# Optimization experiments

Hardware: AMD Instinct MI355X
Metric: run time of the kernel (lower is better)

The kernel has to match this reference:

```python
import jax, jax.numpy as jnp
import numpy as np

NUM_GROUPS = 32
EPS = 1e-5


def group_norm(x, weight, bias):
    # x: [B, C, H, W]; normalize per (group, sample) over channels-in-group and spatial dims
    B, C, H, W = x.shape
    g = x.reshape(B, NUM_GROUPS, C // NUM_GROUPS, H, W)
    mean = g.mean(axis=(2, 3, 4), keepdims=True)
    var = g.var(axis=(2, 3, 4), keepdims=True)
    g = (g - mean) * jax.lax.rsqrt(var + EPS)
    g = g.reshape(B, C, H, W)
    return g * weight[None, :, None, None] + bias[None, :, None, None]


def conv1x1(x, w, b):
    # x: [B, C, H, W], w: [O, C] (1x1 conv kernel squeezed), b: [O]
    return jnp.einsum('bchw,oc->bohw', x, w) + b[None, :, None, None]


def setup_inputs() -> dict:
    key = jax.random.key(0)
    ks = jax.random.split(key, 6)
    B, C, H, W = 16, 512, 64, 64
    scale = 1.0 / np.sqrt(C)
    x = jax.random.normal(ks[0], (B, C, H, W), dtype=jnp.float32)
    return {
        'x': x,
        'gn_weight': jnp.ones((C,), jnp.float32),
        'gn_bias': jnp.zeros((C,), jnp.float32),
        'wq': jax.random.normal(ks[1], (C, C), jnp.float32) * scale,
        'bq': jnp.zeros((C,), jnp.float32),
        'wk': jax.random.normal(ks[2], (C, C), jnp.float32) * scale,
        'bk': jnp.zeros((C,), jnp.float32),
        'wv': jax.random.normal(ks[3], (C, C), jnp.float32) * scale,
        'bv': jnp.zeros((C,), jnp.float32),
        'wo': jax.random.normal(ks[4], (C, C), jnp.float32) * (scale * 1e-5),
        'bo': jnp.zeros((C,), jnp.float32),
    }


def reference(x, gn_weight, gn_bias, wq, bq, wk, bk, wv, bv, wo, bo):
    B, C, H, W = x.shape
    h = group_norm(x, gn_weight, gn_bias)
    q = conv1x1(h, wq, bq)  # [B, C, H, W]
    k = conv1x1(h, wk, bk)
    v = conv1x1(h, wv, bv)
    q = q.transpose(0, 2, 3, 1).reshape(B, H * W, C)   # [B, HW, C]
    kf = k.reshape(B, C, H * W)                        # [B, C, HW]
    w = jnp.einsum('bnc,bcm->bnm', q, kf) * (C ** -0.5)  # [B, HW, HW]
    w = jax.nn.softmax(w, axis=-1)
    vf = v.transpose(0, 2, 3, 1).reshape(B, H * W, C)
    h = jnp.einsum('bnm,bmc->bnc', w, vf)              # [B, HW, C]
    h = h.reshape(B, H, W, C).transpose(0, 3, 1, 2)    # [B, C, H, W]
    h = conv1x1(h, wo, bo)
    return x + h
```

## Files before the change

### kernel.cpp

```cpp
#include <hip/hip_runtime.h>
#include <stdint.h>

typedef __bf16 bf16x8 __attribute__((ext_vector_type(8)));
typedef float  f32x4  __attribute__((ext_vector_type(4)));
typedef unsigned short ushortx8 __attribute__((ext_vector_type(8)));
typedef unsigned short ushortx4 __attribute__((ext_vector_type(4)));

#define DEVI __device__ __forceinline__

DEVI unsigned short f2bf(float f) {
  union { float f; unsigned int u; } v; v.f = f;
  unsigned int r = v.u + 0x7fffu + ((v.u >> 16) & 1u);
  return (unsigned short)(r >> 16);
}
DEVI float bf2f(unsigned short h) {
  union { unsigned int u; float f; } v; v.u = ((unsigned int)h) << 16;
  return v.f;
}

DEVI void gl_lds16(const unsigned short* g, unsigned short* l) {
  __builtin_amdgcn_global_load_lds(
      (__attribute__((address_space(1))) unsigned int*)g,
      (__attribute__((address_space(3))) unsigned int*)l,
      16, 0, 0);
}

DEVI void raw_barrier() {
  asm volatile("" ::: "memory");
  __builtin_amdgcn_s_barrier();
  asm volatile("" ::: "memory");
}
#define WAITCNT_VM4 0x0F74
#define WAITCNT_VM0 0x0F70

DEVI void store_out(float* p, float v) { *p = v; }
DEVI void store_out(unsigned short* p, float v) { *p = f2bf(v); }

__global__ __launch_bounds__(256) void gn_stats(const float* __restrict__ x,
                                                float* __restrict__ stats) {
  const int bg = blockIdx.x;
  const float* p = x + (size_t)bg * 65536;
  const int tid = threadIdx.x;
  float s = 0.f, ss = 0.f;
#pragma unroll 4
  for (int i = 0; i < 64; ++i) {
    float4 v = *(const float4*)(p + (((size_t)i * 256 + tid) << 2));
    s  += v.x + v.y + v.z + v.w;
    ss += v.x * v.x + v.y * v.y + v.z * v.z + v.w * v.w;
  }
  for (int off = 32; off; off >>= 1) { s += __shfl_xor(s, off); ss += __shfl_xor(ss, off); }
  __shared__ float rs[4], rss[4];
  const int lane = tid & 63, wave = tid >> 6;
  if (lane == 0) { rs[wave] = s; rss[wave] = ss; }
  __syncthreads();
  if (tid == 0) {
    float S1 = rs[0] + rs[1] + rs[2] + rs[3];
    float S2 = rss[0] + rss[1] + rss[2] + rss[3];
    float mean = S1 * (1.f / 65536.f);
    float var  = S2 * (1.f / 65536.f) - mean * mean;
    stats[bg * 2 + 0] = mean;
    stats[bg * 2 + 1] = rsqrtf(var + 1e-5f);
  }
}

__global__ __launch_bounds__(256) void gn_apply(const float* __restrict__ x,
                                                const float* __restrict__ stats,
                                                const float* __restrict__ gamma,
                                                const float* __restrict__ beta,
                                                unsigned short* __restrict__ h_t) {
  __shared__ alignas(16) unsigned short tile[64 * 136];
  const int tid = threadIdx.x;
  const int t0 = blockIdx.x * 64;
  const int c0 = blockIdx.y * 128;
  const int b  = blockIdx.z;
  const float* xb = x + ((size_t)b * 512 + c0) * 4096 + t0;
#pragma unroll
  for (int j = 0; j < 8; ++j) {
    int f = tid + j * 256;
    int r = f >> 4;
    int tc = (f & 15) << 2;
    float4 v = *(const float4*)(xb + (size_t)r * 4096 + tc);
    int ch = c0 + r;
    int g = ch >> 4;
    float mean = stats[((size_t)b * 32 + g) * 2 + 0];
    float rstd = stats[((size_t)b * 32 + g) * 2 + 1];
    float ga = gamma[ch] * rstd;
    float be = beta[ch] - mean * ga;
    tile[(tc + 0) * 136 + r] = f2bf(v.x * ga + be);
    tile[(tc + 1) * 136 + r] = f2bf(v.y * ga + be);
    tile[(tc + 2) * 136 + r] = f2bf(v.z * ga + be);
    tile[(tc + 3) * 136 + r] = f2bf(v.w * ga + be);
  }
  __syncthreads();
  unsigned short* hb = h_t + (size_t)b * 4096 * 512;
#pragma unroll
  for (int j = 0; j < 4; ++j) {
    int f = tid + j * 256;
    int tok = f >> 4;
    int cc = (f & 15) << 3;
    ushortx8 v = *(const ushortx8*)&tile[tok * 136 + cc];
    *(ushortx8*)(hb + (size_t)(t0 + tok) * 512 + c0 + cc) = v;
  }
}

__global__ __launch_bounds__(256) void cvt_f32_bf16(const float* __restrict__ s,
                                                    unsigned short* __restrict__ d) {
  int i = (blockIdx.x * 256 + threadIdx.x) * 4;
  float4 v = *(const float4*)(s + i);
  ushortx4 o;
  o[0] = f2bf(v.x); o[1] = f2bf(v.y); o[2] = f2bf(v.z); o[3] = f2bf(v.w);
  *(ushortx4*)(d + i) = o;
}

template <int BIAS_MODE, int RESID, typename OT>
__global__ __launch_bounds__(256) void gemm_nt(
    const unsigned short* __restrict__ A, const unsigned short* __restrict__ B,
    OT* __restrict__ D, const float* __restrict__ bias,
    const float* __restrict__ resid, int M, int N, int K,
    long long sA, long long sB, long long sD, long long sR, float alpha) {
  __shared__ alignas(16) unsigned short As[2][128 * 32];
  __shared__ alignas(16) unsigned short Bs[2][128 * 32];

  const int tid = threadIdx.x;
  const int bz = blockIdx.x, bn = blockIdx.y, bm = blockIdx.z;
  const unsigned short* Ab = A + (size_t)bz * sA + (size_t)bm * 128 * K;
  const unsigned short* Bb = B + (size_t)bz * sB + (size_t)bn * 128 * K;

  const int lane = tid & 63, wave = tid >> 6;
  const int wr = (wave >> 1) * 64, wc = (wave & 1) * 64;
  const int quad = lane >> 4, ln = lane & 15;

  const int r0 = tid >> 2, r1 = (tid + 256) >> 2;
  const int cc = (tid & 3) << 3;

  unsigned short* l0a[2] = { &As[0][(size_t)tid << 3], &As[1][(size_t)tid << 3] };
  unsigned short* l1a[2] = { &As[0][(size_t)(tid + 256) << 3], &As[1][(size_t)(tid + 256) << 3] };
  unsigned short* l0b[2] = { &Bs[0][(size_t)tid << 3], &Bs[1][(size_t)tid << 3] };
  unsigned short* l1b[2] = { &Bs[0][(size_t)(tid + 256) << 3], &Bs[1][(size_t)(tid + 256) << 3] };

  f32x4 acc[4][4] = {};

  const int KT = K >> 5;

  {
    const unsigned short* ag = Ab;
    const unsigned short* bg = Bb;
    gl_lds16(ag + (size_t)r0 * K + cc, l0a[0]);
    gl_lds16(ag + (size_t)r1 * K + cc, l1a[0]);
    gl_lds16(bg + (size_t)r0 * K + cc, l0b[0]);
    gl_lds16(bg + (size_t)r1 * K + cc, l1b[0]);
  }

  int kt = 0;
  for (; kt < KT - 1; ++kt) {
    const int cur = kt & 1, nxt = cur ^ 1;
    {
      const size_t k0 = (size_t)(kt + 1) << 5;
      const unsigned short* ag = Ab + k0;
      const unsigned short* bg = Bb + k0;
      gl_lds16(ag + (size_t)r0 * K + cc, l0a[nxt]);
      gl_lds16(ag + (size_t)r1 * K + cc, l1a[nxt]);
      gl_lds16(bg + (size_t)r0 * K + cc, l0b[nxt]);
      gl_lds16(bg + (size_t)r1 * K + cc, l1b[nxt]);
    }
    __builtin_amdgcn_s_waitcnt(WAITCNT_VM4);
    raw_barrier();

    bf16x8 af[4], bq[4];
#pragma unroll
    for (int mi = 0; mi < 4; ++mi)
      af[mi] = *(const bf16x8*)&As[cur][(wr + mi * 16 + ln) * 32 + quad * 8];
#pragma unroll
    for (int ni = 0; ni < 4; ++ni)
      bq[ni] = *(const bf16x8*)&Bs[cur][(wc + ni * 16 + ln) * 32 + quad * 8];
#pragma unroll
    for (int mi = 0; mi < 4; ++mi)
#pragma unroll
      for (int ni = 0; ni < 4; ++ni)
        acc[mi][ni] = __builtin_amdgcn_mfma_f32_16x16x32_bf16(af[mi], bq[ni],
                                                              acc[mi][ni], 0, 0, 0);
    raw_barrier();
  }

  {
    const int cur = kt & 1;
    __builtin_amdgcn_s_waitcnt(WAITCNT_VM0);
    raw_barrier();
    bf16x8 af[4], bq[4];
#pragma unroll
    for (int mi = 0; mi < 4; ++mi)
      af[mi] = *(const bf16x8*)&As[cur][(wr + mi * 16 + ln) * 32 + quad * 8];
#pragma unroll
    for (int ni = 0; ni < 4; ++ni)
      bq[ni] = *(const bf16x8*)&Bs[cur][(wc + ni * 16 + ln) * 32 + quad * 8];
#pragma unroll
    for (int mi = 0; mi < 4; ++mi)
#pragma unroll
      for (int ni = 0; ni < 4; ++ni)
        acc[mi][ni] = __builtin_amdgcn_mfma_f32_16x16x32_bf16(af[mi], bq[ni],
                                                              acc[mi][ni], 0, 0, 0);
  }

  OT* Db = D + (size_t)bz * sD;
  const float* Rb = RESID ? (resid + (size_t)bz * sR) : nullptr;
#pragma unroll
  for (int mi = 0; mi < 4; ++mi) {
#pragma unroll
    for (int ni = 0; ni < 4; ++ni) {
#pragma unroll
      for (int r = 0; r < 4; ++r) {
        int row = bm * 128 + wr + mi * 16 + quad * 4 + r;
        int col = bn * 128 + wc + ni * 16 + ln;
        float v = acc[mi][ni][r] * alpha;
        if (BIAS_MODE == 1) v += bias[row];
        if (BIAS_MODE == 2) v += bias[col];
        size_t idx = (size_t)row * N + col;
        if (RESID) v += Rb[idx];
        store_out(&Db[idx], v);
      }
    }
  }
}

__global__ __launch_bounds__(256) void softmax_rows(unsigned short* __restrict__ S) {
  const int tid = threadIdx.x;
  unsigned short* p = S + (size_t)blockIdx.x * 4096 + tid * 16;
  ushortx8 u0 = *(const ushortx8*)p;
  ushortx8 u1 = *(const ushortx8*)(p + 8);
  float v[16];
#pragma unroll
  for (int i = 0; i < 8; ++i) { v[i] = bf2f(u0[i]); v[i + 8] = bf2f(u1[i]); }
  float m = v[0];
#pragma unroll
  for (int i = 1; i < 16; ++i) m = fmaxf(m, v[i]);
  for (int off = 32; off; off >>= 1) m = fmaxf(m, __shfl_xor(m, off));
  __shared__ float red[4];
  __shared__ float red2[4];
  const int lane = tid & 63, wave = tid >> 6;
  if (lane == 0) red[wave] = m;
  __syncthreads();
  m = fmaxf(fmaxf(red[0], red[1]), fmaxf(red[2], red[3]));
  float s = 0.f;
#pragma unroll
  for (int i = 0; i < 16; ++i) { v[i] = __expf(v[i] - m); s += v[i]; }
  for (int off = 32; off; off >>= 1) s += __shfl_xor(s, off);
  if (lane == 0) red2[wave] = s;
  __syncthreads();
  s = red2[0] + red2[1] + red2[2] + red2[3];
  float inv = 1.f / s;
#pragma unroll
  for (int i = 0; i < 8; ++i) { u0[i] = f2bf(v[i] * inv); u1[i] = f2bf(v[i + 8] * inv); }
  *(ushortx8*)p = u0;
  *(ushortx8*)(p + 8) = u1;
}

extern "C" void kernel_launch(void* const* d_in, const int* in_sizes, int n_in,
                              void* d_out, int out_size, void* d_ws, size_t ws_size,
                              hipStream_t stream) {
  const float* x   = (const float*)d_in[0];
  const float* gnw = (const float*)d_in[1];
  const float* gnb = (const float*)d_in[2];
  const float* wq  = (const float*)d_in[3];
  const float* bq  = (const float*)d_in[4];
  const float* wk  = (const float*)d_in[5];
  const float* bk  = (const float*)d_in[6];
  const float* wv  = (const float*)d_in[7];
  const float* bv  = (const float*)d_in[8];
  const float* wo  = (const float*)d_in[9];
  const float* bo  = (const float*)d_in[10];
  float* out = (float*)d_out;

  const size_t EB = 2097152;

  char* base = (char*)d_ws;
  unsigned short* h_t  = (unsigned short*)base;
  unsigned short* wqb  = (unsigned short*)(base + 67108864);
  unsigned short* wkb  = wqb + 262144;
  unsigned short* wvb  = wkb + 262144;
  unsigned short* wob  = wvb + 262144;
  float*          stats = (float*)(base + 69206016);
  char*           dyn   = base + 69210112;
  size_t rem = ws_size > 69210112 ? ws_size - 69210112 : 0;

  int nb = 1;
  if      (rem >= (size_t)16 * 46137344) nb = 16;
  else if (rem >= (size_t)8  * 46137344) nb = 8;
  else if (rem >= (size_t)4  * 46137344) nb = 4;
  else if (rem >= (size_t)2  * 46137344) nb = 2;

  unsigned short* q  = (unsigned short*)dyn;
  unsigned short* kb = q  + (size_t)nb * EB;
  unsigned short* vb = kb + (size_t)nb * EB;
  unsigned short* Sb = (unsigned short*)(dyn + (size_t)nb * 3 * 4194304);
  unsigned short* attn = q;

  gn_stats<<<512, 256, 0, stream>>>(x, stats);
  gn_apply<<<dim3(64, 4, 16), 256, 0, stream>>>(x, stats, gnw, gnb, h_t);
  cvt_f32_bf16<<<256, 256, 0, stream>>>(wq, wqb);
  cvt_f32_bf16<<<256, 256, 0, stream>>>(wk, wkb);
  cvt_f32_bf16<<<256, 256, 0, stream>>>(wv, wvb);
  cvt_f32_bf16<<<256, 256, 0, stream>>>(wo, wob);

  const float sm_scale = 0.044194173824159216f;

  for (int b0 = 0; b0 < 16; b0 += nb) {
    const unsigned short* hc = h_t + (size_t)b0 * EB;
    gemm_nt<2, 0, unsigned short><<<dim3(nb, 4, 32), 256, 0, stream>>>(
        hc, wqb, q, bq, nullptr, 4096, 512, 512, (long long)EB, 0, (long long)EB, 0, 1.f);
    gemm_nt<2, 0, unsigned short><<<dim3(nb, 4, 32), 256, 0, stream>>>(
        hc, wkb, kb, bk, nullptr, 4096, 512, 512, (long long)EB, 0, (long long)EB, 0, 1.f);
    gemm_nt<1, 0, unsigned short><<<dim3(nb, 32, 4), 256, 0, stream>>>(
        wvb, hc, vb, bv, nullptr, 512, 4096, 512, 0, (long long)EB, (long long)EB, 0, 1.f);
    gemm_nt<0, 0, unsigned short><<<dim3(nb, 32, 32), 256, 0, stream>>>(
        q, kb, Sb, nullptr, nullptr, 4096, 4096, 512,
        (long long)EB, (long long)EB, 16777216LL, 0, sm_scale);
    softmax_rows<<<nb * 4096, 256, 0, stream>>>(Sb);
    gemm_nt<0, 0, unsigned short><<<dim3(nb, 4, 32), 256, 0, stream>>>(
        Sb, vb, attn, nullptr, nullptr, 4096, 512, 4096,
        16777216LL, (long long)EB, (long long)EB, 0, 1.f);
    gemm_nt<1, 1, float><<<dim3(nb, 32, 4), 256, 0, stream>>>(
        wob, attn, out + (size_t)b0 * EB, bo, x + (size_t)b0 * EB,
        512, 4096, 512, 0, (long long)EB, (long long)EB, (long long)EB, 1.f);
  }
}
```

Measured before the change: 1.522 ms.

## Replace 128x128 GEMM with 256x256-tile 8-wave kernel using swizzled LDS pipeline

```diff
diff --git a/kernel.cpp b/kernel.cpp
--- a/kernel.cpp
+++ b/kernel.cpp
@@ -30,8 +30,9 @@
   __builtin_amdgcn_s_barrier();
   asm volatile("" ::: "memory");
 }
-#define WAITCNT_VM4 0x0F74
-#define WAITCNT_VM0 0x0F70
+#define WAITCNT_VM4    0x0F74
+#define WAITCNT_VM0    0x0F70
+#define WAITCNT_LGKM0  0xC07F
 
 DEVI void store_out(float* p, float v) { *p = v; }
 DEVI void store_out(unsigned short* p, float v) { *p = f2bf(v); }
@@ -113,105 +114,159 @@
 }
 
 template <int BIAS_MODE, int RESID, typename OT>
-__global__ __launch_bounds__(256) void gemm_nt(
+__global__ __launch_bounds__(512, 2) void gemm_nt_256(
     const unsigned short* __restrict__ A, const unsigned short* __restrict__ B,
     OT* __restrict__ D, const float* __restrict__ bias,
     const float* __restrict__ resid, int M, int N, int K,
     long long sA, long long sB, long long sD, long long sR, float alpha) {
-  __shared__ alignas(16) unsigned short As[2][128 * 32];
-  __shared__ alignas(16) unsigned short Bs[2][128 * 32];
+  __shared__ alignas(128) char sm[131072];
+  char* const sA0 = sm;
+  char* const sB0 = sm + 32768;
+  char* const sA1 = sm + 65536;
+  char* const sB1 = sm + 98304;
 
   const int tid = threadIdx.x;
   const int bz = blockIdx.x, bn = blockIdx.y, bm = blockIdx.z;
-  const unsigned short* Ab = A + (size_t)bz * sA + (size_t)bm * 128 * K;
-  const unsigned short* Bb = B + (size_t)bz * sB + (size_t)bn * 128 * K;
-
-  const int lane = tid & 63, wave = tid >> 6;
-  const int wr = (wave >> 1) * 64, wc = (wave & 1) * 64;
-  const int quad = lane >> 4, ln = lane & 15;
-
-  const int r0 = tid >> 2, r1 = (tid + 256) >> 2;
-  const int cc = (tid & 3) << 3;
-
-  unsigned short* l0a[2] = { &As[0][(size_t)tid << 3], &As[1][(size_t)tid << 3] };
-  unsigned short* l1a[2] = { &As[0][(size_t)(tid + 256) << 3], &As[1][(size_t)(tid + 256) << 3] };
-  unsigned short* l0b[2] = { &Bs[0][(size_t)tid << 3], &Bs[1][(size_t)tid << 3] };
-  unsigned short* l1b[2] = { &Bs[0][(size_t)(tid + 256) << 3], &Bs[1][(size_t)(tid + 256) << 3] };
-
-  f32x4 acc[4][4] = {};
-
-  const int KT = K >> 5;
-
+  const unsigned short* Ab = A + (size_t)bz * sA + (size_t)bm * 256 * K;
+  const unsigned short* Bb = B + (size_t)bz * sB + (size_t)bn * 256 * K;
+
+  const int lane = tid & 63;
+  const int ln = lane & 15, quad = lane >> 4;
+  const int wave = tid >> 6;
+  const int wm = wave >> 2, wn = wave & 3;
+
+  const int prow = tid >> 3;
+  const unsigned ks = (unsigned)((tid & 7) ^ (prow & 7));
+  const unsigned srcoff = (unsigned)prow * (unsigned)K + ks * 8u;
+  const unsigned ldst = (unsigned)tid * 16u;
+
+  const int aro = (wm * 128 + ln) * 128;
+  const int bro = (wn * 64 + ln) * 128;
+  const int sl0 = ((quad ^ (ln & 7)) << 4);
+  const int sl1 = (((4 + quad) ^ (ln & 7)) << 4);
+
+  f32x4 acc[8][4] = {};
+  bf16x8 a0[8], a1[8], b0[4], b1[4];
+
+#define STAGE(G, SMp, h, ktv) do {                                                   \
+    const unsigned short* _g = (G) + (unsigned)(h) * 128u * (unsigned)K +            \
+                               (unsigned)(ktv) * 64u + srcoff;                       \
+    gl_lds16(_g, (unsigned short*)((SMp) + (h) * 16384 + ldst));                     \
+    gl_lds16(_g + (size_t)64 * K, (unsigned short*)((SMp) + (h) * 16384 + 8192 + ldst)); \
+  } while (0)
+
+#define RD_A(SMp, SL, dst) do { _Pragma("unroll")                                    \
+    for (int _mf = 0; _mf < 8; ++_mf)                                                \
+      dst[_mf] = *(const bf16x8*)((SMp) + aro + _mf * 2048 + (SL)); } while (0)
+#define RD_B(SMp, SL, dst) do { _Pragma("unroll")                                    \
+    for (int _nf = 0; _nf < 4; ++_nf)                                                \
+      dst[_nf] = *(const bf16x8*)((SMp) + bro + _nf * 2048 + (SL)); } while (0)
+
+#define MM(AF, BF, N0) do {                                                          \
+    __builtin_amdgcn_s_setprio(1);                                                   \
+    _Pragma("unroll")                                                                \
+    for (int _mf = 0; _mf < 8; ++_mf) {                                              \
+      acc[_mf][(N0)]     = __builtin_amdgcn_mfma_f32_16x16x32_bf16(AF[_mf], BF[(N0)],     acc[_mf][(N0)],     0, 0, 0); \
+      acc[_mf][(N0) + 1] = __builtin_amdgcn_mfma_f32_16x16x32_bf16(AF[_mf], BF[(N0) + 1], acc[_mf][(N0) + 1], 0, 0, 0); \
+    }                                                                                \
+    __builtin_amdgcn_s_setprio(0);                                                   \
+  } while (0)
+
+  STAGE(Ab, sA0, 0, 0); STAGE(Ab, sA0, 1, 0);
+  STAGE(Bb, sB0, 0, 0); STAGE(Bb, sB0, 1, 0);
+  STAGE(Ab, sA1, 0, 1); STAGE(Ab, sA1, 1, 1);
+  __builtin_amdgcn_s_waitcnt(WAITCNT_VM4);
+  raw_barrier();
+
+  const int NI = K >> 7;
+  int kt0 = 0;
+  for (int i = 0; i < NI - 1; ++i, kt0 += 2) {
+    RD_A(sA0, sl0, a0); RD_B(sB0, sl0, b0);
+    STAGE(Bb, sB1, 0, kt0 + 1);
+    raw_barrier();
+    MM(a0, b0, 0);
+    raw_barrier();
+    RD_A(sA0, sl1, a1); RD_B(sB0, sl1, b1);
+    STAGE(Bb, sB1, 1, kt0 + 1);
+    raw_barrier();
+    MM(a0, b0, 2);
+    __builtin_amdgcn_s_waitcnt(WAITCNT_LGKM0);
+    raw_barrier();
+    STAGE(Ab, sA0, 0, kt0 + 2);
+    raw_barrier();
+    MM(a1, b1, 0);
+    raw_barrier();
+    STAGE(Ab, sA0, 1, kt0 + 2);
+    raw_barrier();
+    MM(a1, b1, 2);
+    __builtin_amdgcn_s_waitcnt(WAITCNT_VM4);
+    raw_barrier();
+    RD_A(sA1, sl0, a0); RD_B(sB1, sl0, b0);
+    STAGE(Bb, sB0, 0, kt0 + 2);
+    raw_barrier();
+    MM(a0, b0, 0);
+    raw_barrier();
+    RD_A(sA1, sl1, a1); RD_B(sB1, sl1, b1);
+    STAGE(Bb, sB0, 1, kt0 + 2);
+    raw_barrier();
+    MM(a0, b0, 2);
+    __builtin_amdgcn_s_waitcnt(WAITCNT_LGKM0);
+    raw_barrier();
+    STAGE(Ab, sA1, 0, kt0 + 3);
+    raw_barrier();
+    MM(a1, b1, 0);
+    raw_barrier();
+    STAGE(Ab, sA1, 1, kt0 + 3);
+    raw_barrier();
+    MM(a1, b1, 2);
+    __builtin_amdgcn_s_waitcnt(WAITCNT_VM4);
+    raw_barrier();
+  }
   {
-    const unsigned short* ag = Ab;
-    const unsigned short* bg = Bb;
-    gl_lds16(ag + (size_t)r0 * K + cc, l0a[0]);
-    gl_lds16(ag + (size_t)r1 * K + cc, l1a[0]);
-    gl_lds16(bg + (size_t)r0 * K + cc, l0b[0]);
-    gl_lds16(bg + (size_t)r1 * K + cc, l1b[0]);
-  }
-
-  int kt = 0;
-  for (; kt < KT - 1; ++kt) {
-    const int cur = kt & 1, nxt = cur ^ 1;
-    {
-      const size_t k0 = (size_t)(kt + 1) << 5;
-      const unsigned short* ag = Ab + k0;
-      const unsigned short* bg = Bb + k0;
-      gl_lds16(ag + (size_t)r0 * K + cc, l0a[nxt]);
-      gl_lds16(ag + (size_t)r1 * K + cc, l1a[nxt]);
-      gl_lds16(bg + (size_t)r0 * K + cc, l0b[nxt]);
-      gl_lds16(bg + (size_t)r1 * K + cc, l1b[nxt]);
-    }
-    __builtin_amdgcn_s_waitcnt(WAITCNT_VM4);
-    raw_barrier();
-
-    bf16x8 af[4], bq[4];
-#pragma unroll
-    for (int mi = 0; mi < 4; ++mi)
-      af[mi] = *(const bf16x8*)&As[cur][(wr + mi * 16 + ln) * 32 + quad * 8];
-#pragma unroll
-    for (int ni = 0; ni < 4; ++ni)
-      bq[ni] = *(const bf16x8*)&Bs[cur][(wc + ni * 16 + ln) * 32 + quad * 8];
-#pragma unroll
-    for (int mi = 0; mi < 4; ++mi)
-#pragma unroll
-      for (int ni = 0; ni < 4; ++ni)
-        acc[mi][ni] = __builtin_amdgcn_mfma_f32_16x16x32_bf16(af[mi], bq[ni],
-                                                              acc[mi][ni], 0, 0, 0);
-    raw_barrier();
-  }
-
-  {
-    const int cur = kt & 1;
+    RD_A(sA0, sl0, a0); RD_B(sB0, sl0, b0);
+    STAGE(Bb, sB1, 0, kt0 + 1);
+    raw_barrier();
+    MM(a0, b0, 0);
+    raw_barrier();
+    RD_A(sA0, sl1, a1); RD_B(sB0, sl1, b1);
+    STAGE(Bb, sB1, 1, kt0 + 1);
+    raw_barrier();
+    MM(a0, b0, 2);
+    raw_barrier();
+    raw_barrier();
+    MM(a1, b1, 0);
+    raw_barrier();
+    raw_barrier();
+    MM(a1, b1, 2);
     __builtin_amdgcn_s_waitcnt(WAITCNT_VM0);
     raw_barrier();
-    bf16x8 af[4], bq[4];
-#pragma unroll
-    for (int mi = 0; mi < 4; ++mi)
-      af[mi] = *(const bf16x8*)&As[cur][(wr + mi * 16 + ln) * 32 + quad * 8];
-#pragma unroll
-    for (int ni = 0; ni < 4; ++ni)
-      bq[ni] = *(const bf16x8*)&Bs[cur][(wc + ni * 16 + ln) * 32 + quad * 8];
-#pragma unroll
-    for (int mi = 0; mi < 4; ++mi)
-#pragma unroll
-      for (int ni = 0; ni < 4; ++ni)
-        acc[mi][ni] = __builtin_amdgcn_mfma_f32_16x16x32_bf16(af[mi], bq[ni],
-                                                              acc[mi][ni], 0, 0, 0);
-  }
+    RD_A(sA1, sl0, a0); RD_B(sB1, sl0, b0);
+    raw_barrier();
+    MM(a0, b0, 0);
+    raw_barrier();
+    RD_A(sA1, sl1, a1); RD_B(sB1, sl1, b1);
+    raw_barrier();
+    MM(a0, b0, 2);
+    raw_barrier();
+    MM(a1, b1, 0);
+    MM(a1, b1, 2);
+  }
+#undef STAGE
+#undef RD_A
+#undef RD_B
+#undef MM
 
   OT* Db = D + (size_t)bz * sD;
   const float* Rb = RESID ? (resid + (size_t)bz * sR) : nullptr;
 #pragma unroll
-  for (int mi = 0; mi < 4; ++mi) {
-#pragma unroll
-    for (int ni = 0; ni < 4; ++ni) {
+  for (int mf = 0; mf < 8; ++mf) {
+#pragma unroll
+    for (int nf = 0; nf < 4; ++nf) {
 #pragma unroll
       for (int r = 0; r < 4; ++r) {
-        int row = bm * 128 + wr + mi * 16 + quad * 4 + r;
-        int col = bn * 128 + wc + ni * 16 + ln;
-        float v = acc[mi][ni][r] * alpha;
+        int row = bm * 256 + wm * 128 + mf * 16 + quad * 4 + r;
+        int col = bn * 256 + wn * 64 + nf * 16 + ln;
+        float v = acc[mf][nf][r] * alpha;
         if (BIAS_MODE == 1) v += bias[row];
         if (BIAS_MODE == 2) v += bias[col];
         size_t idx = (size_t)row * N + col;
@@ -305,20 +360,20 @@
 
   for (int b0 = 0; b0 < 16; b0 += nb) {
     const unsigned short* hc = h_t + (size_t)b0 * EB;
-    gemm_nt<2, 0, unsigned short><<<dim3(nb, 4, 32), 256, 0, stream>>>(
+    gemm_nt_256<2, 0, unsigned short><<<dim3(nb, 2, 16), 512, 0, stream>>>(
         hc, wqb, q, bq, nullptr, 4096, 512, 512, (long long)EB, 0, (long long)EB, 0, 1.f);
-    gemm_nt<2, 0, unsigned short><<<dim3(nb, 4, 32), 256, 0, stream>>>(
+    gemm_nt_256<2, 0, unsigned short><<<dim3(nb, 2, 16), 512, 0, stream>>>(
         hc, wkb, kb, bk, nullptr, 4096, 512, 512, (long long)EB, 0, (long long)EB, 0, 1.f);
-    gemm_nt<1, 0, unsigned short><<<dim3(nb, 32, 4), 256, 0, stream>>>(
+    gemm_nt_256<1, 0, unsigned short><<<dim3(nb, 16, 2), 512, 0, stream>>>(
         wvb, hc, vb, bv, nullptr, 512, 4096, 512, 0, (long long)EB, (long long)EB, 0, 1.f);
-    gemm_nt<0, 0, unsigned short><<<dim3(nb, 32, 32), 256, 0, stream>>>(
+    gemm_nt_256<0, 0, unsigned short><<<dim3(nb, 16, 16), 512, 0, stream>>>(
         q, kb, Sb, nullptr, nullptr, 4096, 4096, 512,
         (long long)EB, (long long)EB, 16777216LL, 0, sm_scale);
     softmax_rows<<<nb * 4096, 256, 0, stream>>>(Sb);
-    gemm_nt<0, 0, unsigned short><<<dim3(nb, 4, 32), 256, 0, stream>>>(
+    gemm_nt_256<0, 0, unsigned short><<<dim3(nb, 2, 16), 512, 0, stream>>>(
         Sb, vb, attn, nullptr, nullptr, 4096, 512, 4096,
         16777216LL, (long long)EB, (long long)EB, 0, 1.f);
-    gemm_nt<1, 1, float><<<dim3(nb, 32, 4), 256, 0, stream>>>(
+    gemm_nt_256<1, 1, float><<<dim3(nb, 16, 2), 512, 0, stream>>>(
         wob, attn, out + (size_t)b0 * EB, bo, x + (size_t)b0 * EB,
         512, 4096, 512, 0, (long long)EB, (long long)EB, (long long)EB, 1.f);
   }
```

Measured after the change: 1.229 ms. -19.3%, faster.
